# Kernel optimization log

Hardware: AMD Instinct MI355X
Metric: run time of the kernel (lower is better)

Reference implementation:

```python
import jax, jax.numpy as jnp
import numpy as np

NF = 64
G_OFF = 4          # offset groups
K = 9              # 3x3 kernel taps


def lrelu(x):
    return jnp.where(x >= 0, x, 0.1 * x)


def conv3(x, w, b):
    # 3x3 conv, stride 1, pad 1, NCHW / OIHW
    y = jax.lax.conv_general_dilated(
        x, w, window_strides=(1, 1), padding=((1, 1), (1, 1)),
        dimension_numbers=('NCHW', 'OIHW', 'NCHW'))
    return y + b[None, :, None, None]


def deform_conv2d(x, offset, w, b, g_off):
    # torchvision-style DCNv1: 3x3, stride 1, pad 1, weight groups = 1
    B, C, H, W = x.shape
    Cg = C // g_off
    O = w.shape[0]
    # offset layout: [B, 2*g*K, H, W] -> [B, g, K, (dy,dx), H, W]
    off = offset.reshape(B, g_off, K, 2, H, W)
    ky = jnp.repeat(jnp.arange(3), 3).astype(x.dtype)  # kernel row per tap
    kx = jnp.tile(jnp.arange(3), 3).astype(x.dtype)    # kernel col per tap
    py = jnp.arange(H, dtype=x.dtype)[None, :, None] - 1.0 + ky[:, None, None]  # [K,H,1]
    px = jnp.arange(W, dtype=x.dtype)[None, None, :] - 1.0 + kx[:, None, None]  # [K,1,W]
    sy = off[:, :, :, 0] + py[None, None]  # [B,g,K,H,W] sampling rows
    sx = off[:, :, :, 1] + px[None, None]  # [B,g,K,H,W] sampling cols
    y0 = jnp.floor(sy)
    x0 = jnp.floor(sx)
    feat = x.reshape(B, g_off, Cg, H * W)
    acc = jnp.zeros((B, g_off, Cg, K * H * W), dtype=x.dtype)
    for dyc, dxc in ((0.0, 0.0), (0.0, 1.0), (1.0, 0.0), (1.0, 1.0)):
        yc = y0 + dyc
        xc = x0 + dxc
        wgt = (1.0 - jnp.abs(sy - yc)) * (1.0 - jnp.abs(sx - xc))
        valid = (yc >= 0) & (yc < H) & (xc >= 0) & (xc < W)
        wgt = jnp.where(valid, wgt, 0.0)
        idx = (jnp.clip(yc, 0, H - 1).astype(jnp.int32) * W
               + jnp.clip(xc, 0, W - 1).astype(jnp.int32))
        gathered = jnp.take_along_axis(feat, idx.reshape(B, g_off, 1, K * H * W), axis=3)
        acc = acc + gathered * wgt.reshape(B, g_off, 1, K * H * W)
    sampled = acc.reshape(B, C, K, H, W)
    out = jnp.einsum('bckhw,ock->bohw', sampled, w.reshape(O, C, K))
    return out + b[None, :, None, None]


def setup_inputs() -> dict:
    key = jax.random.key(0)
    ks = jax.random.split(key, 16)
    B, H, W = 4, 128, 224
    off_ch = 2 * G_OFF * 9  # 72
    s = 0.05
    inp = {
        'nbr_fea_l': jax.random.normal(ks[0], (B, NF, H, W), jnp.float32),
        'ref_fea_l': jax.random.normal(ks[1], (B, NF, H, W), jnp.float32),
        'w_co1': jax.random.normal(ks[2], (NF, 2 * NF, 3, 3), jnp.float32) * s,
        'b_co1': jnp.zeros((NF,), jnp.float32),
        'w_m1': jax.random.normal(ks[3], (NF, NF, 3, 3), jnp.float32) * s,
        'b_m1': jnp.zeros((NF,), jnp.float32),
        'w_m2': jax.random.normal(ks[4], (NF, NF, 3, 3), jnp.float32) * s,
        'b_m2': jnp.zeros((NF,), jnp.float32),
        'w_m3': jax.random.normal(ks[5], (off_ch, NF, 3, 3), jnp.float32) * 0.01,
        'b_m3': jnp.zeros((off_ch,), jnp.float32),
        'w_dcn': jax.random.normal(ks[6], (NF, NF, 3, 3), jnp.float32) * s,
        'b_dcn': jnp.zeros((NF,), jnp.float32),
    }
    return inp


def reference(nbr_fea_l, ref_fea_l, w_co1, b_co1, w_m1, b_m1, w_m2, b_m2,
              w_m3, b_m3, w_dcn, b_dcn):
    feat = lrelu(conv3(jnp.concatenate([nbr_fea_l, ref_fea_l], axis=1), w_co1, b_co1))
    # MotionNet offset head (assumed 3-layer conv stack)
    off = lrelu(conv3(feat, w_m1, b_m1))
    off = lrelu(conv3(off, w_m2, b_m2))
    off = conv3(off, w_m3, b_m3)  # [B, 2*G*9, H, W]
    return lrelu(deform_conv2d(nbr_fea_l, off, w_dcn, b_dcn, G_OFF))
```

## Files before the change

### kernel.cpp

```cpp
#include <hip/hip_runtime.h>

#define HH 128
#define WW 224
#define HW_ (HH * WW)

typedef short short8 __attribute__((ext_vector_type(8)));
typedef float f32x4 __attribute__((ext_vector_type(4)));
typedef float float2v __attribute__((ext_vector_type(2)));

__device__ __forceinline__ float lrelu_f(float v) { return v >= 0.f ? v : 0.1f * v; }

__device__ __forceinline__ unsigned short f2bf(float f) {
  union { float f; unsigned u; } x; x.f = f;
  unsigned r = x.u + 0x7fff + ((x.u >> 16) & 1);
  return (unsigned short)(r >> 16);
}
__device__ __forceinline__ float bf2f(unsigned short u) {
  union { unsigned u; float f; } x; x.u = ((unsigned)u) << 16; return x.f;
}
__device__ __forceinline__ float asf(unsigned u) {
  union { unsigned u; float f; } x; x.u = u; return x.f;
}

__global__ __launch_bounds__(256)
void prep_xt(const float* __restrict__ nbr, const float* __restrict__ ref,
             unsigned short* __restrict__ xt, unsigned short* __restrict__ xnb) {
  __shared__ __align__(16) char ls[64 * 256];
  const int lane = threadIdx.x & 63;
  const int q = threadIdx.x >> 6;
  const int p0 = blockIdx.x * 64;
  const int p = p0 + lane;
  const int b = blockIdx.y;
  const int c0 = q * 32;
  const float* src = (c0 < 64) ? (nbr + ((size_t)b * 64 + c0) * HW_)
                               : (ref + ((size_t)b * 64 + (c0 - 64)) * HW_);
  unsigned short tmp[32];
  #pragma unroll
  for (int i = 0; i < 32; ++i) tmp[i] = f2bf(src[(size_t)i * HW_ + p]);
  #pragma unroll
  for (int j = 0; j < 4; ++j) {
    const int byte = (c0 * 2 + j * 16) ^ ((lane & 7) << 4);
    *(short8*)(ls + lane * 256 + byte) = *(const short8*)(tmp + j * 8);
  }
  __syncthreads();
  const int tid = threadIdx.x;
  unsigned short* dst = xt + ((size_t)b * HW_ + p0) * 128;
  #pragma unroll
  for (int j = 0; j < 4; ++j) {
    const int unit = tid * 4 + j;
    const int px = unit >> 4, ck = unit & 15;
    const short8 v = *(const short8*)(ls + px * 256 + ((ck * 16) ^ ((px & 7) << 4)));
    *(short8*)(dst + (size_t)px * 128 + ck * 8) = v;
  }
  unsigned short* dst2 = xnb + ((size_t)b * HW_ + p0) * 64;
  #pragma unroll
  for (int j = 0; j < 2; ++j) {
    const int unit = tid * 2 + j;
    const int px = unit >> 3, ck = unit & 7;
    const short8 v = *(const short8*)(ls + px * 256 + ((ck * 16) ^ ((px & 7) << 4)));
    *(short8*)(dst2 + (size_t)px * 64 + ck * 8) = v;
  }
}

__device__ __forceinline__ void wfrag_one(const float* __restrict__ w,
                                          unsigned short* __restrict__ wt,
                                          int i, int O, int C, int NFT) {
  const int CB = C / 32;
  const int j = i & 7;
  const int lane = (i >> 3) & 63;
  const int fid = i >> 9;
  const int nfg = fid % NFT;
  const int kcb = fid / NFT;
  const int cb = kcb % CB;
  const int k = kcb / CB;
  const int o = nfg * 16 + (lane & 15);
  const int c = cb * 32 + (lane >> 4) * 8 + j;
  float v = (o < O) ? w[((size_t)o * C + c) * 9 + k] : 0.f;
  wt[i] = f2bf(v);
}
__device__ __forceinline__ void wdcn_one(const float* __restrict__ w,
                                         unsigned short* __restrict__ wt, int i) {
  const int j = i & 7;
  const int lane = (i >> 3) & 63;
  const int fid = i >> 9;
  const int mf = fid & 3;
  const int s = (fid >> 2) % 5;
  const int g = fid / 20;
  const int l15 = lane & 15, lg = lane >> 4;
  const int o = mf * 16 + l15;
  const int t = 2 * s + (lg >> 1);
  const int c = g * 16 + (lg & 1) * 8 + j;
  float v = (t < 9) ? w[((size_t)o * 64 + c) * 9 + t] : 0.f;
  wt[i] = f2bf(v);
}

__global__ void prep_weights(const float* __restrict__ w1, const float* __restrict__ wm1,
                             const float* __restrict__ wm2, const float* __restrict__ wm3,
                             const float* __restrict__ wdcn,
                             unsigned short* __restrict__ wf1, unsigned short* __restrict__ wfm1,
                             unsigned short* __restrict__ wfm2, unsigned short* __restrict__ wfm3,
                             unsigned short* __restrict__ wdf) {
  int i = blockIdx.x * 256 + threadIdx.x;
  if (i < 73728) { wfrag_one(w1, wf1, i, 64, 128, 4); return; }
  i -= 73728;
  if (i < 36864) { wfrag_one(wm1, wfm1, i, 64, 64, 4); return; }
  i -= 36864;
  if (i < 36864) { wfrag_one(wm2, wfm2, i, 64, 64, 4); return; }
  i -= 36864;
  if (i < 46080) { wfrag_one(wm3, wfm3, i, 72, 64, 5); return; }
  i -= 46080;
  if (i < 40960) wdcn_one(wdcn, wdf, i);
}

template<int CINB, int NFT, int CROW, bool LRELU>
__global__ __launch_bounds__(256, 2)
void conv_lds(const unsigned short* __restrict__ xt, const unsigned short* __restrict__ wfrag,
              const float* __restrict__ bias, unsigned short* __restrict__ out, int coutReal) {
  __shared__ __align__(16) char xs[6 * 34 * 128];
  const int tid = threadIdx.x;
  const int lane = tid & 63, wv = tid >> 6;
  const int l15 = lane & 15, lg = lane >> 4;
  const int b = blockIdx.y;
  const int ty = (blockIdx.x / 7) * 4, tx = (blockIdx.x % 7) * 32;
  const int CIN = CINB * 64;
  const unsigned short* xb = xt + (size_t)b * HW_ * CIN;

  f32x4 acc[2][NFT];
  #pragma unroll
  for (int mf = 0; mf < 2; ++mf)
    #pragma unroll
    for (int nf = 0; nf < NFT; ++nf) acc[mf][nf] = (f32x4){0.f, 0.f, 0.f, 0.f};

  #pragma unroll 1
  for (int cb2 = 0; cb2 < CINB; ++cb2) {
    if (cb2 > 0) __syncthreads();
    for (int ci = tid; ci < 1632; ci += 256) {
      const int ch = ci & 7;
      const int hp = ci >> 3;
      const int hr = hp / 34, hc = hp % 34;
      const int gy = ty + hr - 1, gx = tx + hc - 1;
      short8 v = (short8)0;
      if (((unsigned)gy < HH) & ((unsigned)gx < WW))
        v = *(const short8*)(xb + (size_t)(gy * WW + gx) * CIN + cb2 * 64 + ch * 8);
      *(short8*)(xs + hp * 128 + ((ch * 16) ^ ((hc & 7) << 4))) = v;
    }
    __syncthreads();

    #pragma unroll
    for (int k = 0; k < 9; ++k) {
      const int ky = k / 3, kx = k % 3;
      #pragma unroll
      for (int cb = 0; cb < 2; ++cb) {
        short8 av[2];
        #pragma unroll
        for (int mf = 0; mf < 2; ++mf) {
          const int hr = wv + ky;
          const int hc = mf * 16 + l15 + kx;
          av[mf] = *(const short8*)(xs + (hr * 34 + hc) * 128
                                    + ((cb * 64 + lg * 16) ^ ((hc & 7) << 4)));
        }
        #pragma unroll
        for (int nf = 0; nf < NFT; ++nf) {
          const short8 bv = *(const short8*)(wfrag
              + ((size_t)((k * (CINB * 2) + cb2 * 2 + cb) * NFT + nf)) * 512 + lane * 8);
          #pragma unroll
          for (int mf = 0; mf < 2; ++mf)
            acc[mf][nf] = __builtin_amdgcn_mfma_f32_16x16x32_bf16(av[mf], bv, acc[mf][nf], 0, 0, 0);
        }
      }
    }
  }

  unsigned short* ob = out + (size_t)b * HW_ * CROW;
  const int rr = ty + wv;
  #pragma unroll
  for (int nf = 0; nf < NFT; ++nf) {
    const int o = nf * 16 + l15;
    const bool ov = (o < coutReal);
    const float bz = ov ? bias[o] : 0.f;
    #pragma unroll
    for (int mf = 0; mf < 2; ++mf) {
      #pragma unroll
      for (int r = 0; r < 4; ++r) {
        const int cc = tx + mf * 16 + lg * 4 + r;
        float vv = acc[mf][nf][r] + bz;
        if (LRELU) vv = lrelu_f(vv);
        if (ov) ob[(size_t)(rr * WW + cc) * CROW + o] = f2bf(vv);
      }
    }
  }
}

__global__ __launch_bounds__(256, 2)
void dcn_v6(const unsigned short* __restrict__ xnb,
            const unsigned short* __restrict__ offt,
            const unsigned short* __restrict__ wdf,
            const float* __restrict__ bias, float* __restrict__ out) {
  __shared__ __align__(16) char xs[12 * 24 * 128];
  const int tid = threadIdx.x;
  const int w = tid >> 6, l = tid & 63;
  const int l15 = l & 15, lg = l >> 4;
  const int b = blockIdx.y;
  const int bx = blockIdx.x;
  const int swz = (bx & 7) * 56 + (bx >> 3);
  const int tx = (swz % 14) * 16;
  const int ty = (swz / 14) * 4;
  const int y = ty + w;
  const int x = tx + l15;
  const int p_img = y * WW + x;
  const unsigned short* xb = xnb + (size_t)b * HW_ * 64;

  for (int ci = tid; ci < 2304; ci += 256) {
    const int ch = ci & 7;
    const int pos = ci >> 3;
    const int r = pos / 24, c = pos % 24;
    const int gy = ty - 4 + r, gx = tx - 4 + c;
    short8 v = (short8)0;
    if (((unsigned)gy < HH) & ((unsigned)gx < WW))
      v = *(const short8*)(xb + (size_t)(gy * WW + gx) * 64 + ch * 8);
    *(short8*)(xs + pos * 128 + ((ch * 16) ^ (((r + c) & 7) << 4))) = v;
  }
  __syncthreads();

  const unsigned* od = (const unsigned*)(offt + ((size_t)b * HW_ + p_img) * 72);
  const int thalf = lg >> 1;
  const int cofs0 = (lg & 1) * 8;

  f32x4 acc[4];
  #pragma unroll
  for (int mf = 0; mf < 4; ++mf) acc[mf] = (f32x4){0.f, 0.f, 0.f, 0.f};

  #pragma unroll 1
  for (int g = 0; g < 4; ++g) {
    const int cofs = g * 16 + cofs0;
    const int chunkB = cofs * 2;
    #pragma unroll 1
    for (int s = 0; s < 5; ++s) {
      const int t = 2 * s + thalf;
      const bool live = (t < 9);
      const unsigned dpair = od[g * 9 + (live ? t : 0)];
      const float dy = bf2f((unsigned short)(dpair & 0xffff));
      const float dx = bf2f((unsigned short)(dpair >> 16));
      const float sy = dy + (float)(y - 1 + t / 3);
      const float sx = dx + (float)(x - 1 + t % 3);
      const float fy = floorf(sy);
      const float fx = floorf(sx);
      const int y0 = (int)fy;
      const int x0 = (int)fx;
      const float ay = sy - fy;
      const float ax = sx - fx;
      float w00 = (1.f - ay) * (1.f - ax);
      float w01 = (1.f - ay) * ax;
      float w10 = ay * (1.f - ax);
      float w11 = ay * ax;
      const bool vy0 = (y0 >= 0) & (y0 < HH);
      const bool vy1 = (y0 + 1 >= 0) & (y0 + 1 < HH);
      const bool vx0 = (x0 >= 0) & (x0 < WW);
      const bool vx1 = (x0 + 1 >= 0) & (x0 + 1 < WW);
      w00 = (vy0 & vx0) ? w00 : 0.f;
      w01 = (vy0 & vx1) ? w01 : 0.f;
      w10 = (vy1 & vx0) ? w10 : 0.f;
      w11 = (vy1 & vx1) ? w11 : 0.f;
      const int cy0 = min(max(y0, 0), HH - 1);
      const int cy1 = min(max(y0 + 1, 0), HH - 1);
      const int cx0 = min(max(x0, 0), WW - 1);
      const int cx1 = min(max(x0 + 1, 0), WW - 1);
      const int ry0 = cy0 - ty + 4, ry1 = cy1 - ty + 4;
      const int rx0 = cx0 - tx + 4, rx1 = cx1 - tx + 4;
      const bool inT = !live | (((unsigned)ry0 < 12u) & ((unsigned)ry1 < 12u)
                              & ((unsigned)rx0 < 24u) & ((unsigned)rx1 < 24u));
      short8 q00, q01, q10, q11;
      if (__all((int)inT)) {
        const int a00 = (ry0 * 24 + rx0) * 128 + (chunkB ^ (((ry0 + rx0) & 7) << 4));
        const int a01 = (ry0 * 24 + rx1) * 128 + (chunkB ^ (((ry0 + rx1) & 7) << 4));
        const int a10 = (ry1 * 24 + rx0) * 128 + (chunkB ^ (((ry1 + rx0) & 7) << 4));
        const int a11 = (ry1 * 24 + rx1) * 128 + (chunkB ^ (((ry1 + rx1) & 7) << 4));
        q00 = *(const short8*)(xs + a00);
        q01 = *(const short8*)(xs + a01);
        q10 = *(const short8*)(xs + a10);
        q11 = *(const short8*)(xs + a11);
      } else {
        q00 = *(const short8*)(xb + (size_t)(cy0 * WW + cx0) * 64 + cofs);
        q01 = *(const short8*)(xb + (size_t)(cy0 * WW + cx1) * 64 + cofs);
        q10 = *(const short8*)(xb + (size_t)(cy1 * WW + cx0) * 64 + cofs);
        q11 = *(const short8*)(xb + (size_t)(cy1 * WW + cx1) * 64 + cofs);
      }
      short8 pf = (short8)0;
      if (live) {
        const unsigned* u00 = (const unsigned*)&q00;
        const unsigned* u01 = (const unsigned*)&q01;
        const unsigned* u10 = (const unsigned*)&q10;
        const unsigned* u11 = (const unsigned*)&q11;
        unsigned pr[4];
        #pragma unroll
        for (int i = 0; i < 4; ++i) {
          float2v f00, f01, f10, f11;
          f00.x = asf(u00[i] << 16); f00.y = asf(u00[i] & 0xffff0000u);
          f01.x = asf(u01[i] << 16); f01.y = asf(u01[i] & 0xffff0000u);
          f10.x = asf(u10[i] << 16); f10.y = asf(u10[i] & 0xffff0000u);
          f11.x = asf(u11[i] << 16); f11.y = asf(u11[i] & 0xffff0000u);
          const float2v s2 = f00 * w00 + f01 * w01 + f10 * w10 + f11 * w11;
          unsigned pk;
          asm("v_cvt_pk_bf16_f32 %0, %1, %2" : "=v"(pk) : "v"(s2.x), "v"(s2.y));
          pr[i] = pk;
        }
        pf = *(const short8*)pr;
      }
      #pragma unroll
      for (int mf = 0; mf < 4; ++mf) {
        const short8 wf = *(const short8*)(wdf + ((size_t)((g * 5 + s) * 4 + mf)) * 512 + l * 8);
        acc[mf] = __builtin_amdgcn_mfma_f32_16x16x32_bf16(wf, pf, acc[mf], 0, 0, 0);
      }
    }
  }

  float* ob = out + (size_t)b * 64 * HW_;
  #pragma unroll
  for (int mf = 0; mf < 4; ++mf) {
    #pragma unroll
    for (int r = 0; r < 4; ++r) {
      const int o = mf * 16 + lg * 4 + r;
      ob[(size_t)o * HW_ + p_img] = lrelu_f(acc[mf][r] + bias[o]);
    }
  }
}

extern "C" void kernel_launch(void* const* d_in, const int* in_sizes, int n_in,
                              void* d_out, int out_size, void* d_ws, size_t ws_size,
                              hipStream_t stream) {
  const float* nbr   = (const float*)d_in[0];
  const float* ref   = (const float*)d_in[1];
  const float* w_co1 = (const float*)d_in[2];
  const float* b_co1 = (const float*)d_in[3];
  const float* w_m1  = (const float*)d_in[4];
  const float* b_m1  = (const float*)d_in[5];
  const float* w_m2  = (const float*)d_in[6];
  const float* b_m2  = (const float*)d_in[7];
  const float* w_m3  = (const float*)d_in[8];
  const float* b_m3  = (const float*)d_in[9];
  const float* w_dcn = (const float*)d_in[10];
  const float* b_dcn = (const float*)d_in[11];
  float* out = (float*)d_out;

  char* ws = (char*)d_ws;
  unsigned short* xnb   = (unsigned short*)(ws);
  unsigned short* x1t   = (unsigned short*)(ws + 14680064);
  unsigned short* m1t   = (unsigned short*)(ws + 14680064);
  unsigned short* m2t   = (unsigned short*)(ws + 29360128);
  unsigned short* featt = (unsigned short*)(ws + 44040192);
  unsigned short* offt  = (unsigned short*)(ws + 44040192);
  char* wbase = ws + 60555264;
  unsigned short* wf1  = (unsigned short*)(wbase);
  unsigned short* wfm1 = (unsigned short*)(wbase + 147456);
  unsigned short* wfm2 = (unsigned short*)(wbase + 221184);
  unsigned short* wfm3 = (unsigned short*)(wbase + 294912);
  unsigned short* wdf  = (unsigned short*)(wbase + 387072);

  dim3 blk(256);
  prep_weights<<<dim3(916), blk, 0, stream>>>(w_co1, w_m1, w_m2, w_m3, w_dcn,
                                              wf1, wfm1, wfm2, wfm3, wdf);
  prep_xt<<<dim3(448, 4), blk, 0, stream>>>(nbr, ref, x1t, xnb);

  conv_lds<2, 4, 64, true ><<<dim3(224, 4), blk, 0, stream>>>(x1t,   wf1,  b_co1, featt, 64);
  conv_lds<1, 4, 64, true ><<<dim3(224, 4), blk, 0, stream>>>(featt, wfm1, b_m1,  m1t,   64);
  conv_lds<1, 4, 64, true ><<<dim3(224, 4), blk, 0, stream>>>(m1t,   wfm2, b_m2,  m2t,   64);
  conv_lds<1, 5, 72, false><<<dim3(224, 4), blk, 0, stream>>>(m2t,   wfm3, b_m3,  offt,  72);
  dcn_v6<<<dim3(448, 4), blk, 0, stream>>>(xnb, offt, wdf, b_dcn, out);
}
```

Before: 174.2 us.

## Merge prep kernels, use taller conv tiles, and simplify deformable sampling addressing

Merges the weight-fragment and input-transpose prep kernels into one launch. Adds a conv variant whose tile is 8 rows by 32 columns, with four M-fragments per wave, and uses it for the first three convs. This halves the block count and raises weight-fragment reuse per load, at the cost of more accumulator registers and LDS. In the DCN kernel, per-tap base coordinates are precomputed and the s loop is fully unrolled. Validity masking and clamping are moved to the global-memory fallback path, and the LDS corner addresses are derived from a single base.

```diff
diff --git a/kernel.cpp b/kernel.cpp
--- a/kernel.cpp
+++ b/kernel.cpp
@@ -20,46 +20,6 @@
 }
 __device__ __forceinline__ float asf(unsigned u) {
   union { unsigned u; float f; } x; x.u = u; return x.f;
-}
-
-__global__ __launch_bounds__(256)
-void prep_xt(const float* __restrict__ nbr, const float* __restrict__ ref,
-             unsigned short* __restrict__ xt, unsigned short* __restrict__ xnb) {
-  __shared__ __align__(16) char ls[64 * 256];
-  const int lane = threadIdx.x & 63;
-  const int q = threadIdx.x >> 6;
-  const int p0 = blockIdx.x * 64;
-  const int p = p0 + lane;
-  const int b = blockIdx.y;
-  const int c0 = q * 32;
-  const float* src = (c0 < 64) ? (nbr + ((size_t)b * 64 + c0) * HW_)
-                               : (ref + ((size_t)b * 64 + (c0 - 64)) * HW_);
-  unsigned short tmp[32];
-  #pragma unroll
-  for (int i = 0; i < 32; ++i) tmp[i] = f2bf(src[(size_t)i * HW_ + p]);
-  #pragma unroll
-  for (int j = 0; j < 4; ++j) {
-    const int byte = (c0 * 2 + j * 16) ^ ((lane & 7) << 4);
-    *(short8*)(ls + lane * 256 + byte) = *(const short8*)(tmp + j * 8);
-  }
-  __syncthreads();
-  const int tid = threadIdx.x;
-  unsigned short* dst = xt + ((size_t)b * HW_ + p0) * 128;
-  #pragma unroll
-  for (int j = 0; j < 4; ++j) {
-    const int unit = tid * 4 + j;
-    const int px = unit >> 4, ck = unit & 15;
-    const short8 v = *(const short8*)(ls + px * 256 + ((ck * 16) ^ ((px & 7) << 4)));
-    *(short8*)(dst + (size_t)px * 128 + ck * 8) = v;
-  }
-  unsigned short* dst2 = xnb + ((size_t)b * HW_ + p0) * 64;
-  #pragma unroll
-  for (int j = 0; j < 2; ++j) {
-    const int unit = tid * 2 + j;
-    const int px = unit >> 3, ck = unit & 7;
-    const short8 v = *(const short8*)(ls + px * 256 + ((ck * 16) ^ ((px & 7) << 4)));
-    *(short8*)(dst2 + (size_t)px * 64 + ck * 8) = v;
-  }
 }
 
 __device__ __forceinline__ void wfrag_one(const float* __restrict__ w,
@@ -94,22 +54,143 @@
   wt[i] = f2bf(v);
 }
 
-__global__ void prep_weights(const float* __restrict__ w1, const float* __restrict__ wm1,
-                             const float* __restrict__ wm2, const float* __restrict__ wm3,
-                             const float* __restrict__ wdcn,
-                             unsigned short* __restrict__ wf1, unsigned short* __restrict__ wfm1,
-                             unsigned short* __restrict__ wfm2, unsigned short* __restrict__ wfm3,
-                             unsigned short* __restrict__ wdf) {
-  int i = blockIdx.x * 256 + threadIdx.x;
-  if (i < 73728) { wfrag_one(w1, wf1, i, 64, 128, 4); return; }
-  i -= 73728;
-  if (i < 36864) { wfrag_one(wm1, wfm1, i, 64, 64, 4); return; }
-  i -= 36864;
-  if (i < 36864) { wfrag_one(wm2, wfm2, i, 64, 64, 4); return; }
-  i -= 36864;
-  if (i < 46080) { wfrag_one(wm3, wfm3, i, 72, 64, 5); return; }
-  i -= 46080;
-  if (i < 40960) wdcn_one(wdcn, wdf, i);
+__global__ __launch_bounds__(256)
+void prep_all(const float* __restrict__ nbr, const float* __restrict__ ref,
+              const float* __restrict__ w1, const float* __restrict__ wm1,
+              const float* __restrict__ wm2, const float* __restrict__ wm3,
+              const float* __restrict__ wdcn,
+              unsigned short* __restrict__ xt, unsigned short* __restrict__ xnb,
+              unsigned short* __restrict__ wf1, unsigned short* __restrict__ wfm1,
+              unsigned short* __restrict__ wfm2, unsigned short* __restrict__ wfm3,
+              unsigned short* __restrict__ wdf) {
+  __shared__ __align__(16) char ls[64 * 256];
+  if (blockIdx.x >= 1792) {
+    int i = (blockIdx.x - 1792) * 256 + threadIdx.x;
+    if (i < 73728) { wfrag_one(w1, wf1, i, 64, 128, 4); return; }
+    i -= 73728;
+    if (i < 36864) { wfrag_one(wm1, wfm1, i, 64, 64, 4); return; }
+    i -= 36864;
+    if (i < 36864) { wfrag_one(wm2, wfm2, i, 64, 64, 4); return; }
+    i -= 36864;
+    if (i < 46080) { wfrag_one(wm3, wfm3, i, 72, 64, 5); return; }
+    i -= 46080;
+    if (i < 40960) wdcn_one(wdcn, wdf, i);
+    return;
+  }
+  const int lane = threadIdx.x & 63;
+  const int q = threadIdx.x >> 6;
+  const int bxp = blockIdx.x % 448;
+  const int b = blockIdx.x / 448;
+  const int p0 = bxp * 64;
+  const int p = p0 + lane;
+  const int c0 = q * 32;
+  const float* src = (c0 < 64) ? (nbr + ((size_t)b * 64 + c0) * HW_)
+                               : (ref + ((size_t)b * 64 + (c0 - 64)) * HW_);
+  unsigned short tmp[32];
+  #pragma unroll
+  for (int i = 0; i < 32; ++i) tmp[i] = f2bf(src[(size_t)i * HW_ + p]);
+  #pragma unroll
+  for (int j = 0; j < 4; ++j) {
+    const int byte = (c0 * 2 + j * 16) ^ ((lane & 7) << 4);
+    *(short8*)(ls + lane * 256 + byte) = *(const short8*)(tmp + j * 8);
+  }
+  __syncthreads();
+  const int tid = threadIdx.x;
+  unsigned short* dst = xt + ((size_t)b * HW_ + p0) * 128;
+  #pragma unroll
+  for (int j = 0; j < 4; ++j) {
+    const int unit = tid * 4 + j;
+    const int px = unit >> 4, ck = unit & 15;
+    const short8 v = *(const short8*)(ls + px * 256 + ((ck * 16) ^ ((px & 7) << 4)));
+    *(short8*)(dst + (size_t)px * 128 + ck * 8) = v;
+  }
+  unsigned short* dst2 = xnb + ((size_t)b * HW_ + p0) * 64;
+  #pragma unroll
+  for (int j = 0; j < 2; ++j) {
+    const int unit = tid * 2 + j;
+    const int px = unit >> 3, ck = unit & 7;
+    const short8 v = *(const short8*)(ls + px * 256 + ((ck * 16) ^ ((px & 7) << 4)));
+    *(short8*)(dst2 + (size_t)px * 64 + ck * 8) = v;
+  }
+}
+
+template<int CINB, int NFT, int CROW, bool LRELU>
+__global__ __launch_bounds__(256, 2)
+void conv_lds2(const unsigned short* __restrict__ xt, const unsigned short* __restrict__ wfrag,
+               const float* __restrict__ bias, unsigned short* __restrict__ out, int coutReal) {
+  __shared__ __align__(16) char xs[10 * 34 * 128];
+  const int tid = threadIdx.x;
+  const int lane = tid & 63, wv = tid >> 6;
+  const int l15 = lane & 15, lg = lane >> 4;
+  const int b = blockIdx.y;
+  const int ty = (blockIdx.x / 7) * 8, tx = (blockIdx.x % 7) * 32;
+  const int CIN = CINB * 64;
+  const unsigned short* xb = xt + (size_t)b * HW_ * CIN;
+
+  f32x4 acc[4][NFT];
+  #pragma unroll
+  for (int mf = 0; mf < 4; ++mf)
+    #pragma unroll
+    for (int nf = 0; nf < NFT; ++nf) acc[mf][nf] = (f32x4){0.f, 0.f, 0.f, 0.f};
+
+  #pragma unroll 1
+  for (int cb2 = 0; cb2 < CINB; ++cb2) {
+    if (cb2 > 0) __syncthreads();
+    for (int ci = tid; ci < 2720; ci += 256) {
+      const int ch = ci & 7;
+      const int hp = ci >> 3;
+      const int hr = hp / 34, hc = hp % 34;
+      const int gy = ty + hr - 1, gx = tx + hc - 1;
+      short8 v = (short8)0;
+      if (((unsigned)gy < HH) & ((unsigned)gx < WW))
+        v = *(const short8*)(xb + (size_t)(gy * WW + gx) * CIN + cb2 * 64 + ch * 8);
+      *(short8*)(xs + hp * 128 + ((ch * 16) ^ ((hc & 7) << 4))) = v;
+    }
+    __syncthreads();
+
+    #pragma unroll
+    for (int k = 0; k < 9; ++k) {
+      const int ky = k / 3, kx = k % 3;
+      #pragma unroll
+      for (int cb = 0; cb < 2; ++cb) {
+        short8 av[4];
+        #pragma unroll
+        for (int mf = 0; mf < 4; ++mf) {
+          const int hr = 2 * wv + (mf >> 1) + ky;
+          const int hc = (mf & 1) * 16 + l15 + kx;
+          av[mf] = *(const short8*)(xs + (hr * 34 + hc) * 128
+                                    + ((cb * 64 + lg * 16) ^ ((hc & 7) << 4)));
+        }
+        #pragma unroll
+        for (int nf = 0; nf < NFT; ++nf) {
+          const short8 bv = *(const short8*)(wfrag
+              + ((size_t)((k * (CINB * 2) + cb2 * 2 + cb) * NFT + nf)) * 512 + lane * 8);
+          #pragma unroll
+          for (int mf = 0; mf < 4; ++mf)
+            acc[mf][nf] = __builtin_amdgcn_mfma_f32_16x16x32_bf16(av[mf], bv, acc[mf][nf], 0, 0, 0);
+        }
+      }
+    }
+  }
+
+  unsigned short* ob = out + (size_t)b * HW_ * CROW;
+  #pragma unroll
+  for (int nf = 0; nf < NFT; ++nf) {
+    const int o = nf * 16 + l15;
+    const bool ov = (o < coutReal);
+    const float bz = ov ? bias[o] : 0.f;
+    #pragma unroll
+    for (int mf = 0; mf < 4; ++mf) {
+      const int rr = ty + 2 * wv + (mf >> 1);
+      #pragma unroll
+      for (int r = 0; r < 4; ++r) {
+        const int cc = tx + (mf & 1) * 16 + lg * 4 + r;
+        float vv = acc[mf][nf][r] + bz;
+        if (LRELU) vv = lrelu_f(vv);
+        if (ov) ob[(size_t)(rr * WW + cc) * CROW + o] = f2bf(vv);
+      }
+    }
+  }
 }
 
 template<int CINB, int NFT, int CROW, bool LRELU>
@@ -192,7 +273,7 @@
 }
 
 __global__ __launch_bounds__(256, 2)
-void dcn_v6(const unsigned short* __restrict__ xnb,
+void dcn_v7(const unsigned short* __restrict__ xnb,
             const unsigned short* __restrict__ offt,
             const unsigned short* __restrict__ wdf,
             const float* __restrict__ bias, float* __restrict__ out) {
@@ -226,6 +307,17 @@
   const int thalf = lg >> 1;
   const int cofs0 = (lg & 1) * 8;
 
+  float pyA[5], pxA[5];
+  int liveA[5];
+  #pragma unroll
+  for (int s = 0; s < 5; ++s) {
+    const int t = 2 * s + thalf;
+    liveA[s] = (t < 9);
+    const int tt = liveA[s] ? t : 0;
+    pyA[s] = (float)(y - 1 + tt / 3);
+    pxA[s] = (float)(x - 1 + tt % 3);
+  }
+
   f32x4 acc[4];
   #pragma unroll
   for (int mf = 0; mf < 4; ++mf) acc[mf] = (f32x4){0.f, 0.f, 0.f, 0.f};
@@ -234,52 +326,53 @@
   for (int g = 0; g < 4; ++g) {
     const int cofs = g * 16 + cofs0;
     const int chunkB = cofs * 2;
-    #pragma unroll 1
+    #pragma unroll
     for (int s = 0; s < 5; ++s) {
+      const int live = liveA[s];
       const int t = 2 * s + thalf;
-      const bool live = (t < 9);
       const unsigned dpair = od[g * 9 + (live ? t : 0)];
       const float dy = bf2f((unsigned short)(dpair & 0xffff));
       const float dx = bf2f((unsigned short)(dpair >> 16));
-      const float sy = dy + (float)(y - 1 + t / 3);
-      const float sx = dx + (float)(x - 1 + t % 3);
+      const float sy = dy + pyA[s];
+      const float sx = dx + pxA[s];
       const float fy = floorf(sy);
       const float fx = floorf(sx);
       const int y0 = (int)fy;
       const int x0 = (int)fx;
       const float ay = sy - fy;
       const float ax = sx - fx;
-      float w00 = (1.f - ay) * (1.f - ax);
-      float w01 = (1.f - ay) * ax;
-      float w10 = ay * (1.f - ax);
-      float w11 = ay * ax;
-      const bool vy0 = (y0 >= 0) & (y0 < HH);
-      const bool vy1 = (y0 + 1 >= 0) & (y0 + 1 < HH);
-      const bool vx0 = (x0 >= 0) & (x0 < WW);
-      const bool vx1 = (x0 + 1 >= 0) & (x0 + 1 < WW);
-      w00 = (vy0 & vx0) ? w00 : 0.f;
-      w01 = (vy0 & vx1) ? w01 : 0.f;
-      w10 = (vy1 & vx0) ? w10 : 0.f;
-      w11 = (vy1 & vx1) ? w11 : 0.f;
-      const int cy0 = min(max(y0, 0), HH - 1);
-      const int cy1 = min(max(y0 + 1, 0), HH - 1);
-      const int cx0 = min(max(x0, 0), WW - 1);
-      const int cx1 = min(max(x0 + 1, 0), WW - 1);
-      const int ry0 = cy0 - ty + 4, ry1 = cy1 - ty + 4;
-      const int rx0 = cx0 - tx + 4, rx1 = cx1 - tx + 4;
-      const bool inT = !live | (((unsigned)ry0 < 12u) & ((unsigned)ry1 < 12u)
-                              & ((unsigned)rx0 < 24u) & ((unsigned)rx1 < 24u));
+      const float by = 1.f - ay, bxx = 1.f - ax;
+      float w00 = by * bxx, w01 = by * ax, w10 = ay * bxx, w11 = ay * ax;
+      const int ry0 = y0 - ty + 4;
+      const int rx0 = x0 - tx + 4;
+      const bool inT = (!live) | (((unsigned)ry0 < 11u) & ((unsigned)rx0 < 23u));
       short8 q00, q01, q10, q11;
       if (__all((int)inT)) {
-        const int a00 = (ry0 * 24 + rx0) * 128 + (chunkB ^ (((ry0 + rx0) & 7) << 4));
-        const int a01 = (ry0 * 24 + rx1) * 128 + (chunkB ^ (((ry0 + rx1) & 7) << 4));
-        const int a10 = (ry1 * 24 + rx0) * 128 + (chunkB ^ (((ry1 + rx0) & 7) << 4));
-        const int a11 = (ry1 * 24 + rx1) * 128 + (chunkB ^ (((ry1 + rx1) & 7) << 4));
-        q00 = *(const short8*)(xs + a00);
-        q01 = *(const short8*)(xs + a01);
-        q10 = *(const short8*)(xs + a10);
-        q11 = *(const short8*)(xs + a11);
+        const int r0 = live ? ry0 : 0;
+        const int c0 = live ? rx0 : 0;
+        const int b00 = (r0 * 24 + c0) << 7;
+        const int sw00 = b00 + (chunkB ^ (((r0 + c0) & 7) << 4));
+        const int sw01 = b00 + 128 + (chunkB ^ (((r0 + c0 + 1) & 7) << 4));
+        const int b10 = b00 + 24 * 128;
+        const int sw10 = b10 + (chunkB ^ (((r0 + c0 + 1) & 7) << 4));
+        const int sw11 = b10 + 128 + (chunkB ^ (((r0 + c0 + 2) & 7) << 4));
+        q00 = *(const short8*)(xs + sw00);
+        q01 = *(const short8*)(xs + sw01);
+        q10 = *(const short8*)(xs + sw10);
+        q11 = *(const short8*)(xs + sw11);
       } else {
+        const bool vy0 = (y0 >= 0) & (y0 < HH);
+        const bool vy1 = (y0 + 1 >= 0) & (y0 + 1 < HH);
+        const bool vx0 = (x0 >= 0) & (x0 < WW);
+        const bool vx1 = (x0 + 1 >= 0) & (x0 + 1 < WW);
+        w00 = (vy0 & vx0) ? w00 : 0.f;
+        w01 = (vy0 & vx1) ? w01 : 0.f;
+        w10 = (vy1 & vx0) ? w10 : 0.f;
+        w11 = (vy1 & vx1) ? w11 : 0.f;
+        const int cy0 = min(max(y0, 0), HH - 1);
+        const int cy1 = min(max(y0 + 1, 0), HH - 1);
+        const int cx0 = min(max(x0, 0), WW - 1);
+        const int cx1 = min(max(x0 + 1, 0), WW - 1);
         q00 = *(const short8*)(xb + (size_t)(cy0 * WW + cx0) * 64 + cofs);
         q01 = *(const short8*)(xb + (size_t)(cy0 * WW + cx1) * 64 + cofs);
         q10 = *(const short8*)(xb + (size_t)(cy1 * WW + cx0) * 64 + cofs);
@@ -357,13 +450,12 @@
   unsigned short* wdf  = (unsigned short*)(wbase + 387072);
 
   dim3 blk(256);
-  prep_weights<<<dim3(916), blk, 0, stream>>>(w_co1, w_m1, w_m2, w_m3, w_dcn,
-                                              wf1, wfm1, wfm2, wfm3, wdf);
-  prep_xt<<<dim3(448, 4), blk, 0, stream>>>(nbr, ref, x1t, xnb);
-
-  conv_lds<2, 4, 64, true ><<<dim3(224, 4), blk, 0, stream>>>(x1t,   wf1,  b_co1, featt, 64);
-  conv_lds<1, 4, 64, true ><<<dim3(224, 4), blk, 0, stream>>>(featt, wfm1, b_m1,  m1t,   64);
-  conv_lds<1, 4, 64, true ><<<dim3(224, 4), blk, 0, stream>>>(m1t,   wfm2, b_m2,  m2t,   64);
-  conv_lds<1, 5, 72, false><<<dim3(224, 4), blk, 0, stream>>>(m2t,   wfm3, b_m3,  offt,  72);
-  dcn_v6<<<dim3(448, 4), blk, 0, stream>>>(xnb, offt, wdf, b_dcn, out);
-}
+  prep_all<<<dim3(2708), blk, 0, stream>>>(nbr, ref, w_co1, w_m1, w_m2, w_m3, w_dcn,
+                                           x1t, xnb, wf1, wfm1, wfm2, wfm3, wdf);
+
+  conv_lds2<2, 4, 64, true ><<<dim3(112, 4), blk, 0, stream>>>(x1t,   wf1,  b_co1, featt, 64);
+  conv_lds2<1, 4, 64, true ><<<dim3(112, 4), blk, 0, stream>>>(featt, wfm1, b_m1,  m1t,   64);
+  conv_lds2<1, 4, 64, true ><<<dim3(112, 4), blk, 0, stream>>>(m1t,   wfm2, b_m2,  m2t,   64);
+  conv_lds <1, 5, 72, false><<<dim3(224, 4), blk, 0, stream>>>(m2t,   wfm3, b_m3,  offt,  72);
+  dcn_v7<<<dim3(448, 4), blk, 0, stream>>>(xnb, offt, wdf, b_dcn, out);
+}
```

Result: faster. 167.1 us (-4.1%).
